# Kernel tuning notes

Hardware: AMD Instinct MI355X
Metric: run time of the kernel (lower is better)

Reference implementation:

```python
import jax, jax.numpy as jnp
import numpy as np
from jax import lax

SIGMA = 2.0      # init arg
HIGH = 0.2       # init arg: high_threshold
LOW = 0.1        # skimage canny default low_threshold for float images
MAX_ITERS = 256  # cap for hysteresis propagation


def _conv2(img, kern):
    # img (N,1,H,W), kern (kh,kw); reflect-padded 'same' convolution
    kh, kw = kern.shape
    p = jnp.pad(img, ((0, 0), (0, 0), (kh // 2, kh // 2), (kw // 2, kw // 2)), mode='reflect')
    k = kern[None, None].astype(img.dtype)
    return lax.conv_general_dilated(p, k, (1, 1), 'VALID')


def _canny(x):
    # x (N,1,H,W) in [0,1] -> binary edge maps (N,H,W) float32
    r = int(4.0 * SIGMA + 0.5)
    g1 = np.exp(-0.5 * (np.arange(-r, r + 1) / SIGMA) ** 2)
    g1 = (g1 / g1.sum()).astype(np.float32)
    # separable gaussian blur
    sm = _conv2(_conv2(x, jnp.asarray(g1[:, None])), jnp.asarray(g1[None, :]))
    # sobel gradients
    sob = jnp.asarray([[-1., 0., 1.], [-2., 0., 2.], [-1., 0., 1.]], jnp.float32)
    gx = _conv2(sm, sob)[:, 0]
    gy = _conv2(sm, sob.T)[:, 0]          # (N,H,W)
    mag = jnp.hypot(gx, gy)
    ang = jnp.degrees(jnp.arctan2(gy, gx)) % 180.0
    N, H, W = mag.shape
    mp = jnp.pad(mag, ((0, 0), (1, 1), (1, 1)))
    sh = lambda dy, dx: mp[:, 1 + dy:1 + dy + H, 1 + dx:1 + dx + W]
    # quantize gradient direction into 4 bins for non-max suppression
    b0 = (ang < 22.5) | (ang >= 157.5)            # horizontal gradient -> E/W neighbors
    b1 = (ang >= 22.5) & (ang < 67.5)             # 45 deg
    b2 = (ang >= 67.5) & (ang < 112.5)            # vertical
    n1 = jnp.where(b0, sh(0, 1), jnp.where(b1, sh(-1, 1), jnp.where(b2, sh(-1, 0), sh(-1, -1))))
    n2 = jnp.where(b0, sh(0, -1), jnp.where(b1, sh(1, -1), jnp.where(b2, sh(1, 0), sh(1, 1))))
    keep = (mag >= n1) & (mag >= n2)
    strong = keep & (mag > HIGH)
    weak = keep & (mag > LOW)

    def dilate(s):
        f = lax.reduce_window(s.astype(jnp.float32), -jnp.inf, lax.max, (1, 3, 3), (1, 1, 1), 'SAME')
        return f > 0.0

    # hysteresis: propagate strong labels through weak pixels until fixpoint
    def cond(c):
        return c[1] & (c[2] < MAX_ITERS)

    def body(c):
        s, _, it = c
        ns = (dilate(s) & weak) | s
        return ns, jnp.any(ns != s), it + 1

    strong, _, _ = lax.while_loop(cond, body, (strong, jnp.array(True), jnp.array(0, jnp.int32)))
    return strong.astype(jnp.float32)


def setup_inputs() -> dict:
    key = jax.random.key(0)
    k1, k2, k3 = jax.random.split(key, 3)
    N, H, W = 16, 1024, 1024
    x = jax.random.uniform(k1, (N, 1, H, W), jnp.float32)
    y = jax.random.uniform(k2, (N, 1, H, W), jnp.float32)
    mask = jax.random.uniform(k3, (H, W), jnp.float32)
    return {"x": x, "y": y, "mask": mask}


def reference(x, y, mask):
    # original detaches x before canny -> edges carry no gradient
    edges = lax.stop_gradient(_canny(x))          # (N,H,W)
    # sum over batch of per-sample mean L1 (nn.L1Loss default reduction='mean')
    diff = jnp.abs(edges * mask - y[:, 0] * mask)
    return jnp.sum(jnp.mean(diff, axis=(1, 2)))
```

## Files before the change

kernel.cpp:

```cpp
#include <hip/hip_runtime.h>
#include <cmath>

#define IMG_W   1024
#define IMG_H   1024
#define NIMG    16
#define HW      (1024 * 1024)
#define NHW     (16 * 1024 * 1024)
#define WPR     16
#define WPI     (IMG_H * WPR)

struct GW { float w[9]; };

__device__ __forceinline__ int refl(int v) {
    return v < 0 ? -v : (v > 1023 ? 2046 - v : v);
}

__global__ void blur_v(const float* __restrict__ in, float* __restrict__ out, GW g) {
    int gid = blockIdx.x * 256 + threadIdx.x;
    int c4  = gid & 255;
    int rc  = (gid >> 8) & 127;
    const float* img = in  + (size_t)(gid >> 15) * HW;
    float*      outp = out + (size_t)(gid >> 15) * HW;
    int y0 = rc * 8;
    float4 acc[8];
#pragma unroll
    for (int j = 0; j < 8; ++j) acc[j] = make_float4(0.f, 0.f, 0.f, 0.f);
#pragma unroll
    for (int d = -8; d <= 15; ++d) {
        int rr = refl(y0 + d);
        float4 v = *(const float4*)(img + rr * IMG_W + c4 * 4);
#pragma unroll
        for (int j = 0; j < 8; ++j) {
            int k = d - j;
            if (k >= -8 && k <= 8) {
                float wt = g.w[k < 0 ? -k : k];
                acc[j].x += wt * v.x; acc[j].y += wt * v.y;
                acc[j].z += wt * v.z; acc[j].w += wt * v.w;
            }
        }
    }
#pragma unroll
    for (int j = 0; j < 8; ++j)
        *(float4*)(outp + (y0 + j) * IMG_W + c4 * 4) = acc[j];
}

__global__ void __launch_bounds__(256, 5)
hgradnms(const float* __restrict__ vb, unsigned long long* __restrict__ strongw,
         unsigned long long* __restrict__ weakw, GW g) {
    __shared__ float L[68 * 88];
    unsigned char* Bn = (unsigned char*)(L + 66 * 68);

    int tid = threadIdx.x;
    int b   = blockIdx.x;
    int img = b >> 8;
    int tr  = (b >> 4) & 15, tc = b & 15;
    int r0  = tr * 64, c0 = tc * 64;
    const float* vimg = vb + (size_t)img * HW;

    if (tc > 0 && tc < 15) {
        const float* basep = vimg + (c0 - 12);
        for (int i = tid; i < 68 * 22; i += 256) {
            int l = i / 22, q = i % 22;
            int gr = refl(r0 + l - 2);
            *(float4*)(L + l * 88 + 4 * q) = *(const float4*)(basep + gr * IMG_W + 4 * q);
        }
    } else {
        for (int i = tid; i < 68 * 88; i += 256) {
            int l = i / 88, m = i % 88;
            int gr = refl(r0 + l - 2);
            int gc = refl(c0 - 12 + m);
            L[i] = vimg[gr * IMG_W + gc];
        }
    }
    __syncthreads();

    float4 oreg[5];
#pragma unroll
    for (int it = 0; it < 5; ++it) {
        int i = tid + it * 256;
        if (i < 68 * 17) {
            int l = i / 17, gq = i % 17;
            float w24[24];
#pragma unroll
            for (int q = 0; q < 6; ++q)
                ((float4*)w24)[q] = *(const float4*)(L + l * 88 + 4 * gq + 4 * q);
            float o0 = 0.f, o1 = 0.f, o2 = 0.f, o3 = 0.f;
#pragma unroll
            for (int t = 0; t < 17; ++t) {
                float wt = g.w[t < 8 ? 8 - t : t - 8];
                o0 += wt * w24[2 + t]; o1 += wt * w24[3 + t];
                o2 += wt * w24[4 + t]; o3 += wt * w24[5 + t];
            }
            oreg[it] = make_float4(o0, o1, o2, o3);
        }
    }
    __syncthreads();
#pragma unroll
    for (int it = 0; it < 5; ++it) {
        int i = tid + it * 256;
        if (i < 68 * 17) {
            int l = i / 17, gq = i % 17;
            *(float4*)(L + l * 88 + 4 * gq) = oreg[it];
        }
    }
    __syncthreads();

    const float T1 = 0.41421356237309503f;
    const float T2 = 2.41421356237309510f;
    float4 mreg[5];
    unsigned int breg[5];
#pragma unroll
    for (int it = 0; it < 5; ++it) {
        int i = tid + it * 256;
        if (i < 66 * 17) {
            int row = i / 17, gq = i % 17;
            float ra[8], rb[8], rc8[8];
            ((float4*)ra)[0]  = *(const float4*)(L + (row    ) * 88 + 4 * gq);
            ((float4*)ra)[1]  = *(const float4*)(L + (row    ) * 88 + 4 * gq + 4);
            ((float4*)rb)[0]  = *(const float4*)(L + (row + 1) * 88 + 4 * gq);
            ((float4*)rb)[1]  = *(const float4*)(L + (row + 1) * 88 + 4 * gq + 4);
            ((float4*)rc8)[0] = *(const float4*)(L + (row + 2) * 88 + 4 * gq);
            ((float4*)rc8)[1] = *(const float4*)(L + (row + 2) * 88 + 4 * gq + 4);
            int pr = r0 + row - 1;
            bool rin = (unsigned)pr <= 1023u;
            float mv[4]; unsigned int bpk = 0;
#pragma unroll
            for (int j = 0; j < 4; ++j) {
                int colidx = 4 * gq + j;
                float a00 = ra[j], a01 = ra[j + 1], a02 = ra[j + 2];
                float a10 = rb[j],                   a12 = rb[j + 2];
                float a20 = rc8[j], a21 = rc8[j + 1], a22 = rc8[j + 2];
                float gx = (a02 - a00) + 2.f * (a12 - a10) + (a22 - a20);
                float gy = (a20 + 2.f * a21 + a22) - (a00 + 2.f * a01 + a02);
                int pc = c0 + colidx - 1;
                bool in = rin && ((unsigned)pc <= 1023u) && (colidx <= 65);
                mv[j] = in ? sqrtf(gx * gx + gy * gy) : 0.f;
                float ax = fabsf(gx), ay = fabsf(gy);
                int bn;
                if (ay < T1 * ax)      bn = 0;
                else if (ay > T2 * ax) bn = 2;
                else                   bn = ((gx > 0.f) == (gy > 0.f)) ? 1 : 3;
                bpk |= (unsigned)bn << (8 * j);
            }
            mreg[it] = make_float4(mv[0], mv[1], mv[2], mv[3]);
            breg[it] = bpk;
        }
    }
    __syncthreads();
#pragma unroll
    for (int it = 0; it < 5; ++it) {
        int i = tid + it * 256;
        if (i < 66 * 17) {
            int row = i / 17, gq = i % 17;
            *(float4*)(L + row * 68 + 4 * gq) = mreg[it];
            *(unsigned int*)(Bn + row * 68 + 4 * gq) = breg[it];
        }
    }
    __syncthreads();

    int lane = tid & 63, wv = tid >> 6;
    unsigned long long* sgw = strongw + (size_t)img * WPI;
    unsigned long long* wkw = weakw   + (size_t)img * WPI;
    for (int it = 0; it < 16; ++it) {
        int qr = wv * 16 + it;
        int qc = lane;
        float cm = L[(qr + 1) * 68 + qc + 1];
        int bn = Bn[(qr + 1) * 68 + qc + 1];
        int d1y = (bn == 0) ? 0 : -1;
        int d1x = (bn < 2) ? 1 : ((bn == 2) ? 0 : -1);
        float n1 = L[(qr + 1 + d1y) * 68 + (qc + 1 + d1x)];
        float n2 = L[(qr + 1 - d1y) * 68 + (qc + 1 - d1x)];
        bool keep   = (cm >= n1) && (cm >= n2);
        bool strong = keep && (cm > 0.2f);
        bool weak   = keep && (cm > 0.1f);
        unsigned long long sb = __ballot(strong);
        unsigned long long wb = __ballot(weak);
        if (lane == 0) {
            int widx = (r0 + qr) * WPR + tc;
            sgw[widx] = sb;
            wkw[widx] = wb;
        }
    }
}

__global__ void __launch_bounds__(1024, 1)
hyst(unsigned long long* __restrict__ strongw, const unsigned long long* __restrict__ weakw) {
    __shared__ unsigned long long S[WPI];
    __shared__ int chg;
    unsigned long long* sg = strongw + (size_t)blockIdx.x * WPI;
    const unsigned long long* wk = weakw + (size_t)blockIdx.x * WPI;
    int t = threadIdx.x;
    int c = t & 15;
    int rbase = (t >> 4) * 16;

    unsigned long long ww[16];
#pragma unroll
    for (int i = 0; i < 16; ++i) {
        S[(rbase + i) * WPR + c] = sg[(rbase + i) * WPR + c];
        ww[i] = wk[(rbase + i) * WPR + c];
    }
    __syncthreads();

    for (int pass = 0; pass < 4096; ++pass) {
        if (t == 0) chg = 0;
        __syncthreads();
        int any = 0;
        auto step = [&](int r, unsigned long long wwv) {
            unsigned long long w = S[r * WPR + c];
            if (!(wwv & ~w)) return;
            unsigned long long up = 0, dn = 0, upl = 0, upr = 0, dnl = 0, dnr = 0, ml = 0, mr = 0;
            if (r > 0)    { up = S[(r - 1) * WPR + c];
                            if (c > 0)  upl = S[(r - 1) * WPR + c - 1];
                            if (c < 15) upr = S[(r - 1) * WPR + c + 1]; }
            if (r < 1023) { dn = S[(r + 1) * WPR + c];
                            if (c > 0)  dnl = S[(r + 1) * WPR + c - 1];
                            if (c < 15) dnr = S[(r + 1) * WPR + c + 1]; }
            if (c > 0)  ml = S[r * WPR + c - 1];
            if (c < 15) mr = S[r * WPR + c + 1];
            unsigned long long H =
                  up | (up << 1) | (up >> 1) | (upl >> 63) | (upr << 63)
                | w  | (w  << 1) | (w  >> 1) | (ml  >> 63) | (mr  << 63)
                | dn | (dn << 1) | (dn >> 1) | (dnl >> 63) | (dnr << 63);
            unsigned long long nw = w | (H & wwv);
            for (;;) {
                unsigned long long nn = nw | (((nw << 1) | (nw >> 1)) & wwv);
                if (nn == nw) break;
                nw = nn;
            }
            if (nw != w) { S[r * WPR + c] = nw; any = 1; }
        };
        if (!(pass & 1)) {
#pragma unroll
            for (int i = 0; i < 16; ++i) step(rbase + i, ww[i]);
        } else {
#pragma unroll
            for (int i = 15; i >= 0; --i) step(rbase + i, ww[i]);
        }
        if (any) chg = 1;
        __syncthreads();
        int done = (chg == 0);
        __syncthreads();
        if (done) break;
    }
#pragma unroll
    for (int i = 0; i < 16; ++i) sg[(rbase + i) * WPR + c] = S[(rbase + i) * WPR + c];
}

__global__ void loss_part(const unsigned long long* __restrict__ strongw,
                          const float* __restrict__ y, const float* __restrict__ mask,
                          float* __restrict__ part) {
    int tid = threadIdx.x;
    float local = 0.f;
    const float4* y4 = (const float4*)y;
    const float4* m4 = (const float4*)mask;
    for (int i4 = blockIdx.x * 256 + tid; i4 < NHW / 4; i4 += 2048 * 256) {
        unsigned long long wword = strongw[i4 >> 4];
        int sh = (i4 & 15) * 4;
        unsigned bits = (unsigned)((wword >> sh) & 0xFull);
        float4 yv = y4[i4];
        float4 mv = m4[i4 & (HW / 4 - 1)];
        local += fabsf(((bits & 1u) ? mv.x : 0.f) - yv.x * mv.x);
        local += fabsf(((bits & 2u) ? mv.y : 0.f) - yv.y * mv.y);
        local += fabsf(((bits & 4u) ? mv.z : 0.f) - yv.z * mv.z);
        local += fabsf(((bits & 8u) ? mv.w : 0.f) - yv.w * mv.w);
    }
    for (int off = 32; off; off >>= 1) local += __shfl_down(local, off);
    __shared__ float wsum[4];
    if ((tid & 63) == 0) wsum[tid >> 6] = local;
    __syncthreads();
    if (tid == 0) part[blockIdx.x] = wsum[0] + wsum[1] + wsum[2] + wsum[3];
}

__global__ void loss_final(const float* __restrict__ part, float* __restrict__ out) {
    int tid = threadIdx.x;
    double s = 0.0;
    for (int i = tid; i < 2048; i += 256) s += (double)part[i];
    for (int off = 32; off; off >>= 1) s += __shfl_down(s, off);
    __shared__ double ws4[4];
    if ((tid & 63) == 0) ws4[tid >> 6] = s;
    __syncthreads();
    if (tid == 0) out[0] = (float)((ws4[0] + ws4[1] + ws4[2] + ws4[3]) * (1.0 / (double)HW));
}

extern "C" void kernel_launch(void* const* d_in, const int* in_sizes, int n_in,
                              void* d_out, int out_size, void* d_ws, size_t ws_size,
                              hipStream_t stream) {
    const float* x    = (const float*)d_in[0];
    const float* y    = (const float*)d_in[1];
    const float* mask = (const float*)d_in[2];
    float* out = (float*)d_out;

    char* ws = (char*)d_ws;
    float* vbuf = (float*)(ws);
    unsigned long long* strongw = (unsigned long long*)(ws + (size_t)64 * 1024 * 1024);
    unsigned long long* weakw   = (unsigned long long*)(ws + (size_t)66 * 1024 * 1024);
    float* part = (float*)(ws + (size_t)68 * 1024 * 1024);

    GW g;
    {
        double e[9], s;
        for (int k = 0; k < 9; ++k) e[k] = std::exp(-0.5 * (k / 2.0) * (k / 2.0));
        s = e[0];
        for (int k = 1; k < 9; ++k) s += 2.0 * e[k];
        for (int k = 0; k < 9; ++k) g.w[k] = (float)(e[k] / s);
    }

    blur_v    <<<2048, 256, 0, stream>>>(x, vbuf, g);
    hgradnms  <<<4096, 256, 0, stream>>>(vbuf, strongw, weakw, g);
    hyst      <<<NIMG, 1024, 0, stream>>>(strongw, weakw);
    loss_part <<<2048, 256, 0, stream>>>(strongw, y, mask, part);
    loss_final<<<1, 256, 0, stream>>>(part, out);
}
```

Measured before the change: 339.4 us.

## Pre-propagate hysteresis in per-strip blocks before whole-image pass

Adds a hyst_strip kernel that splits each image into 16 row strips of 64 rows, each handled by its own block with one halo row above and below. Two strip launches run before the existing single-block-per-image hysteresis, so most propagation happens across 256 blocks instead of 16. This should cut the iteration count of the serial whole-image pass. The cost is two extra launches and extra global traffic; the final hyst pass still guarantees the fixpoint.

```diff
diff --git a/kernel.cpp b/kernel.cpp
--- a/kernel.cpp
+++ b/kernel.cpp
@@ -181,6 +181,61 @@
             wkw[widx] = wb;
         }
     }
+}
+
+__global__ void __launch_bounds__(1024, 1)
+hyst_strip(unsigned long long* __restrict__ strongw, const unsigned long long* __restrict__ weakw) {
+    __shared__ unsigned long long S[66 * WPR];
+    __shared__ int chg;
+    int img = blockIdx.x >> 4, st = blockIdx.x & 15;
+    int r0 = st * 64;
+    unsigned long long* sg = strongw + (size_t)img * WPI;
+    const unsigned long long* wk = weakw + (size_t)img * WPI;
+    int t = threadIdx.x;
+    int c = t & 15, lr = t >> 4;
+    int r = lr + 1;
+
+    S[r * WPR + c] = sg[(r0 + lr) * WPR + c];
+    unsigned long long ww = wk[(r0 + lr) * WPR + c];
+    if (t < WPR)
+        S[t] = (r0 > 0) ? sg[(r0 - 1) * WPR + t] : 0ull;
+    else if (t < 2 * WPR)
+        S[65 * WPR + (t - WPR)] = (r0 + 64 < IMG_H) ? sg[(r0 + 64) * WPR + (t - WPR)] : 0ull;
+    __syncthreads();
+
+    for (int pass = 0; pass < 512; ++pass) {
+        if (t == 0) chg = 0;
+        __syncthreads();
+        int any = 0;
+        unsigned long long w = S[r * WPR + c];
+        if (ww & ~w) {
+            unsigned long long up = S[(r - 1) * WPR + c];
+            unsigned long long dn = S[(r + 1) * WPR + c];
+            unsigned long long upl = (c > 0)  ? S[(r - 1) * WPR + c - 1] : 0ull;
+            unsigned long long upr = (c < 15) ? S[(r - 1) * WPR + c + 1] : 0ull;
+            unsigned long long dnl = (c > 0)  ? S[(r + 1) * WPR + c - 1] : 0ull;
+            unsigned long long dnr = (c < 15) ? S[(r + 1) * WPR + c + 1] : 0ull;
+            unsigned long long ml  = (c > 0)  ? S[r * WPR + c - 1] : 0ull;
+            unsigned long long mr  = (c < 15) ? S[r * WPR + c + 1] : 0ull;
+            unsigned long long H =
+                  up | (up << 1) | (up >> 1) | (upl >> 63) | (upr << 63)
+                | w  | (w  << 1) | (w  >> 1) | (ml  >> 63) | (mr  << 63)
+                | dn | (dn << 1) | (dn >> 1) | (dnl >> 63) | (dnr << 63);
+            unsigned long long nw = w | (H & ww);
+            for (;;) {
+                unsigned long long nn = nw | (((nw << 1) | (nw >> 1)) & ww);
+                if (nn == nw) break;
+                nw = nn;
+            }
+            if (nw != w) { S[r * WPR + c] = nw; any = 1; }
+        }
+        if (any) chg = 1;
+        __syncthreads();
+        int done = (chg == 0);
+        __syncthreads();
+        if (done) break;
+    }
+    sg[(r0 + lr) * WPR + c] = S[r * WPR + c];
 }
 
 __global__ void __launch_bounds__(1024, 1)
@@ -307,6 +362,8 @@
 
     blur_v    <<<2048, 256, 0, stream>>>(x, vbuf, g);
     hgradnms  <<<4096, 256, 0, stream>>>(vbuf, strongw, weakw, g);
+    hyst_strip<<<NIMG * 16, 1024, 0, stream>>>(strongw, weakw);
+    hyst_strip<<<NIMG * 16, 1024, 0, stream>>>(strongw, weakw);
     hyst      <<<NIMG, 1024, 0, stream>>>(strongw, weakw);
     loss_part <<<2048, 256, 0, stream>>>(strongw, y, mask, part);
     loss_final<<<1, 256, 0, stream>>>(part, out);
```

After: 322.8 us. 4.9% less time.
